# Kernel optimization log

Hardware: AMD Instinct MI355X
Metric: run time of the kernel (lower is better)

Reference implementation:

```python
import jax, jax.numpy as jnp
import numpy as np
import math

B, S, D, H = 4, 2048, 1024, 16
HD = D // H  # head_size = 64


def setup_inputs() -> dict:
    key = jax.random.key(0)
    ks = jax.random.split(key, 12)
    s = 1.0 / math.sqrt(D)
    inp = {
        "query_in": jax.random.normal(ks[0], (B, S, D), jnp.float32),
        "key_in": jax.random.normal(ks[1], (B, S, D), jnp.float32),
        "values_in": jax.random.normal(ks[2], (B, S, D), jnp.float32),
        # causal mask, broadcast over batch and heads
        "mask": jnp.tril(jnp.ones((S, S), jnp.int32))[None, None],
        "Wq": jax.random.normal(ks[3], (D, D), jnp.float32) * s,
        "bq": jnp.zeros((D,), jnp.float32),
        "Wk": jax.random.normal(ks[4], (D, D), jnp.float32) * s,
        "bk": jnp.zeros((D,), jnp.float32),
        "Wv": jax.random.normal(ks[5], (D, D), jnp.float32) * s,
        "bv": jnp.zeros((D,), jnp.float32),
        "Wo": jax.random.normal(ks[6], (D, D), jnp.float32) * s,
        "bo": jnp.zeros((D,), jnp.float32),
    }
    return inp


def _heads(x):
    # [B,S,D] -> [B,H,S,HD]
    return x.reshape(B, S, H, HD).transpose(0, 2, 1, 3)


def reference(query_in, key_in, values_in, mask, Wq, bq, Wk, bk, Wv, bv, Wo, bo):
    q = _heads(query_in @ Wq.T + bq)
    k = _heads(key_in @ Wk.T + bk)
    v = _heads(values_in @ Wv.T + bv)
    # scaled dot-product scores [B,H,Sq,Sk]
    att = jnp.einsum("bhqd,bhkd->bhqk", q, k) / math.sqrt(HD)
    att = jnp.where(mask == 0, jnp.float32(-1e9), att)
    # NOTE: original module applies dropout (identity at eval / p=0) directly
    # to scores with NO softmax -- faithfully reproduced here.
    out = jnp.einsum("bhqk,bhkd->bhqd", att, v)
    out = out.transpose(0, 2, 1, 3).reshape(B, S, D)
    return out @ Wo.T + bo
```

## Files before the change

kernel.cpp:

```cpp
#include <hip/hip_runtime.h>
#include <stdint.h>

typedef unsigned short ushort_t;
typedef __bf16 bf16x8 __attribute__((ext_vector_type(8)));
typedef float f32x4 __attribute__((ext_vector_type(4)));
typedef ushort_t us4 __attribute__((ext_vector_type(4)));

#define MFMA16(a, b, c) __builtin_amdgcn_mfma_f32_16x16x32_bf16((a), (b), (c), 0, 0, 0)

constexpr int Bn = 4, Sn = 2048, Dn = 1024, Hn = 16, HDn = 64;
constexpr float SCALE = 0.125f;
constexpr float NEG = -1e9f;

__device__ __forceinline__ float bf2f(ushort_t u) {
  unsigned x = ((unsigned)u) << 16;
  return __builtin_bit_cast(float, x);
}
__device__ __forceinline__ ushort_t f2bf(float f) {
  unsigned x = __builtin_bit_cast(unsigned, f);
  x = x + 0x7FFFu + ((x >> 16) & 1u);
  return (ushort_t)(x >> 16);
}
__device__ __forceinline__ uint4 ld8_f32_bf16(const float* __restrict__ p) {
  float4 a = *(const float4*)p;
  float4 b = *(const float4*)(p + 4);
  union { ushort_t u[8]; uint4 v; } r;
  r.u[0] = f2bf(a.x); r.u[1] = f2bf(a.y); r.u[2] = f2bf(a.z); r.u[3] = f2bf(a.w);
  r.u[4] = f2bf(b.x); r.u[5] = f2bf(b.y); r.u[6] = f2bf(b.z); r.u[7] = f2bf(b.w);
  return r.v;
}
__device__ __forceinline__ void gl2lds16(const void* g, void* l) {
  __builtin_amdgcn_global_load_lds(
      (__attribute__((address_space(1))) void*)g,
      (__attribute__((address_space(3))) void*)l, 16, 0, 0);
}

__global__ __launch_bounds__(256)
void cvt_all(const float* __restrict__ xq, const float* __restrict__ xk,
             const float* __restrict__ xv, const float* __restrict__ wq,
             const float* __restrict__ wk, const float* __restrict__ wv,
             const float* __restrict__ wo, ushort_t* __restrict__ Xd,
             ushort_t* __restrict__ Wd) {
  const int bid = blockIdx.x;
  if (bid < 12288) {
    const int which = bid >> 12;
    const float* s = which == 0 ? xq : which == 1 ? xk : xv;
    size_t i = ((size_t)(bid & 4095) * 256 + threadIdx.x) * 8;
    *(uint4*)(Xd + (size_t)which * 8388608 + i) = ld8_f32_bf16(s + i);
  } else {
    const int wb = bid - 12288, which = wb >> 9;
    const float* s = which == 0 ? wq : which == 1 ? wk : which == 2 ? wv : wo;
    size_t i = ((size_t)(wb & 511) * 256 + threadIdx.x) * 8;
    *(uint4*)(Wd + (size_t)which * 1048576 + i) = ld8_f32_bf16(s + i);
  }
}

__global__ __launch_bounds__(256, 4)
void gemm_qkv(const ushort_t* __restrict__ Xb, const ushort_t* __restrict__ Wb,
              const float* __restrict__ bq, const float* __restrict__ bk,
              const float* __restrict__ bv, ushort_t* __restrict__ Qd,
              ushort_t* __restrict__ Ktd, ushort_t* __restrict__ Vtd) {
  constexpr int K = 1024;
  __shared__ __align__(16) ushort_t As[128 * 64];
  __shared__ __align__(16) ushort_t Bs[128 * 64];

  const int z = blockIdx.z;
  const ushort_t* A  = Xb + (size_t)z * 8388608;
  const ushort_t* Wt = Wb + (size_t)z * 1048576;
  const float* bias = z == 0 ? bq : z == 1 ? bk : bv;
  ushort_t* Cp = z == 0 ? Qd : z == 1 ? Ktd : Vtd;

  const int tid = threadIdx.x;
  const int lane = tid & 63, w = tid >> 6;
  const int quad = lane >> 4, l16 = lane & 15;
  const int wm = w >> 1, wn = w & 1;
  const int row0 = blockIdx.x * 128;
  const int col0 = blockIdx.y * 128;

  const int sr = lane >> 3;
  const int sg = ((lane & 7) ^ (sr & 7)) * 8;
  const ushort_t* Ab = A  + (size_t)(row0 + w * 32 + sr) * K + sg;
  const ushort_t* Bb = Wt + (size_t)(col0 + w * 32 + sr) * K + sg;

  f32x4 acc[4][4] = {};

  for (int k0 = 0; k0 < K; k0 += 64) {
    __syncthreads();
#pragma unroll
    for (int i = 0; i < 4; ++i) {
      gl2lds16(Ab + (size_t)(i * 8) * K + k0, &As[(w * 32 + i * 8) * 64]);
      gl2lds16(Bb + (size_t)(i * 8) * K + k0, &Bs[(w * 32 + i * 8) * 64]);
    }
    __syncthreads();
#pragma unroll
    for (int ks = 0; ks < 2; ++ks) {
      const int kg = ((ks * 4 + quad) ^ (l16 & 7)) * 8;
      bf16x8 af[4], bfr[4];
#pragma unroll
      for (int mt = 0; mt < 4; ++mt)
        af[mt] = *(const bf16x8*)(&As[(wm * 64 + mt * 16 + l16) * 64 + kg]);
#pragma unroll
      for (int nt = 0; nt < 4; ++nt)
        bfr[nt] = *(const bf16x8*)(&Bs[(wn * 64 + nt * 16 + l16) * 64 + kg]);
#pragma unroll
      for (int mt = 0; mt < 4; ++mt)
#pragma unroll
        for (int nt = 0; nt < 4; ++nt)
          acc[mt][nt] = MFMA16(af[mt], bfr[nt], acc[mt][nt]);
    }
  }

#pragma unroll
  for (int mt = 0; mt < 4; ++mt) {
#pragma unroll
    for (int nt = 0; nt < 4; ++nt) {
      const int col = col0 + wn * 64 + nt * 16 + l16;
      const float bv4 = bias[col];
      const int rowb = row0 + wm * 64 + mt * 16 + quad * 4;
      if (z != 0) {
        const int b = rowb >> 11, s = rowb & (Sn - 1);
        const int h = col >> 6, hd = col & 63;
        us4 pk;
#pragma unroll
        for (int r = 0; r < 4; ++r) pk[r] = f2bf(acc[mt][nt][r] + bv4);
        *(us4*)(Cp + ((size_t)((b * Hn + h) * HDn + hd)) * Sn + s) = pk;
      } else {
#pragma unroll
        for (int r = 0; r < 4; ++r) {
          const int row = rowb + r;
          const int b = row >> 11, s = row & (Sn - 1);
          const int h = col >> 6, hd = col & 63;
          Cp[(((size_t)(b * Hn + h) * Sn + s) << 6) + hd] = f2bf(acc[mt][nt][r] + bv4);
        }
      }
    }
  }
}

__global__ __launch_bounds__(256, 4)
void gemm_out(const ushort_t* __restrict__ A, const ushort_t* __restrict__ Wt,
              const float* __restrict__ bias, float* __restrict__ Cp) {
  constexpr int K = 1024;
  __shared__ __align__(16) ushort_t As[128 * 64];
  __shared__ __align__(16) ushort_t Bs[128 * 64];

  const int tid = threadIdx.x;
  const int lane = tid & 63, w = tid >> 6;
  const int quad = lane >> 4, l16 = lane & 15;
  const int wm = w >> 1, wn = w & 1;
  const int row0 = blockIdx.x * 128;
  const int col0 = blockIdx.y * 128;

  const int sr = lane >> 3;
  const int sg = ((lane & 7) ^ (sr & 7)) * 8;
  const ushort_t* Ab = A  + (size_t)(row0 + w * 32 + sr) * K + sg;
  const ushort_t* Bb = Wt + (size_t)(col0 + w * 32 + sr) * K + sg;

  f32x4 acc[4][4] = {};

  for (int k0 = 0; k0 < K; k0 += 64) {
    __syncthreads();
#pragma unroll
    for (int i = 0; i < 4; ++i) {
      gl2lds16(Ab + (size_t)(i * 8) * K + k0, &As[(w * 32 + i * 8) * 64]);
      gl2lds16(Bb + (size_t)(i * 8) * K + k0, &Bs[(w * 32 + i * 8) * 64]);
    }
    __syncthreads();
#pragma unroll
    for (int ks = 0; ks < 2; ++ks) {
      const int kg = ((ks * 4 + quad) ^ (l16 & 7)) * 8;
      bf16x8 af[4], bfr[4];
#pragma unroll
      for (int mt = 0; mt < 4; ++mt)
        af[mt] = *(const bf16x8*)(&As[(wm * 64 + mt * 16 + l16) * 64 + kg]);
#pragma unroll
      for (int nt = 0; nt < 4; ++nt)
        bfr[nt] = *(const bf16x8*)(&Bs[(wn * 64 + nt * 16 + l16) * 64 + kg]);
#pragma unroll
      for (int mt = 0; mt < 4; ++mt)
#pragma unroll
        for (int nt = 0; nt < 4; ++nt)
          acc[mt][nt] = MFMA16(af[mt], bfr[nt], acc[mt][nt]);
    }
  }

#pragma unroll
  for (int mt = 0; mt < 4; ++mt)
#pragma unroll
    for (int nt = 0; nt < 4; ++nt) {
      const int col = col0 + wn * 64 + nt * 16 + l16;
      const float bv = bias[col];
      const int rowb = row0 + wm * 64 + mt * 16 + quad * 4;
#pragma unroll
      for (int r = 0; r < 4; ++r)
        Cp[(size_t)(rowb + r) * 1024 + col] = acc[mt][nt][r] + bv;
    }
}

__global__ __launch_bounds__(256)
void prefixz(const ushort_t* __restrict__ Kt, const ushort_t* __restrict__ Vt,
             ushort_t* __restrict__ Zp, float* __restrict__ suffV) {
  __shared__ __align__(16) ushort_t Kts[2][4096];
  __shared__ __align__(16) ushort_t Vts[2][4096];
  __shared__ float tsum[32 * 64];
  const int tid = threadIdx.x, lane = tid & 63, w = tid >> 6;
  const int quad = lane >> 4, l16 = lane & 15;
  const int bh = blockIdx.x;
  const ushort_t* Ktb = Kt + (size_t)bh * HDn * Sn;
  const ushort_t* Vtb = Vt + (size_t)bh * HDn * Sn;

  const int sr = lane >> 3;
  const int sg = ((lane & 7) ^ (sr & 7)) * 8;

  for (int i = tid; i < 2048; i += 256) tsum[i] = 0.f;

#pragma unroll
  for (int c = 0; c < 2; ++c) {
    const int row = w * 16 + c * 8;
    gl2lds16(Ktb + (size_t)(row + sr) * Sn + sg, &Kts[0][row * 64]);
    gl2lds16(Vtb + (size_t)(row + sr) * Sn + sg, &Vts[0][row * 64]);
  }

  f32x4 zacc[4] = {};

  for (int t = 0; t < 32; ++t) {
    const int cur = t & 1;
    __syncthreads();
    if (t < 31) {
#pragma unroll
      for (int c = 0; c < 2; ++c) {
        const int row = w * 16 + c * 8;
        gl2lds16(Ktb + (size_t)(row + sr) * Sn + (t + 1) * 64 + sg, &Kts[1 - cur][row * 64]);
        gl2lds16(Vtb + (size_t)(row + sr) * Sn + (t + 1) * 64 + sg, &Vts[1 - cur][row * 64]);
      }
    }
    ushort_t* zd = Zp + (size_t)(bh * 32 + t) * 4096;
#pragma unroll
    for (int nt = 0; nt < 4; ++nt) {
      us4 pk;
#pragma unroll
      for (int r = 0; r < 4; ++r) pk[r] = f2bf(SCALE * zacc[nt][r]);
      *(us4*)(zd + (nt * 16 + l16) * 64 + w * 16 + quad * 4) = pk;
    }
    if (t < 31) {
#pragma unroll
      for (int ks = 0; ks < 2; ++ks) {
        const int kg = ((ks * 4 + quad) ^ (l16 & 7)) * 8;
        bf16x8 ak = *(const bf16x8*)(&Kts[cur][(w * 16 + l16) * 64 + kg]);
#pragma unroll
        for (int nt = 0; nt < 4; ++nt) {
          bf16x8 bv8 = *(const bf16x8*)(&Vts[cur][(nt * 16 + l16) * 64 + kg]);
          zacc[nt] = MFMA16(ak, bv8, zacc[nt]);
        }
      }
    }
    {
      const int n = tid & 63, j = tid >> 6;
      float p = 0.f;
#pragma unroll
      for (int gg2 = 0; gg2 < 2; ++gg2) {
        const int g = 2 * j + gg2;
        union { uint4 v; ushort_t u[8]; } c;
        c.v = *(const uint4*)(&Vts[cur][n * 64 + ((g ^ (n & 7)) << 3)]);
#pragma unroll
        for (int e = 0; e < 8; ++e) p += bf2f(c.u[e]);
      }
      atomicAdd(&tsum[t * 64 + n], p);
    }
  }
  __syncthreads();
  if (tid < 64) {
    float acc = 0.f;
    for (int t = 31; t >= 0; --t) {
      suffV[(size_t)(bh * 32 + t) * 64 + tid] = acc;
      acc += tsum[t * 64 + tid];
    }
  }
}

__global__ __launch_bounds__(256)
void attn_kernel(const ushort_t* __restrict__ Q, const ushort_t* __restrict__ Kt,
                 const ushort_t* __restrict__ Vt, const ushort_t* __restrict__ Zp,
                 const float* __restrict__ suffV, ushort_t* __restrict__ O) {
  __shared__ __align__(16) ushort_t Qs[2][4096];
  __shared__ __align__(16) ushort_t Vts[2][4096];
  __shared__ __align__(16) ushort_t Zs[2][4096];
  __shared__ __align__(16) ushort_t Ks[2][4096];
  __shared__ __align__(16) ushort_t Ss[64][72];

  const int tid = threadIdx.x, lane = tid & 63, w = tid >> 6;
  const int quad = lane >> 4, l16 = lane & 15;
  const int bh = blockIdx.x;
  const int qtb = blockIdx.y * 4;
  const int b = bh >> 4, h = bh & 15;
  const ushort_t* Qb  = Q  + (size_t)bh * Sn * HDn;
  const ushort_t* Ktb = Kt + (size_t)bh * HDn * Sn;
  const ushort_t* Vtb = Vt + (size_t)bh * HDn * Sn;

  const int sr = lane >> 3;
  const int sg = ((lane & 7) ^ (sr & 7)) * 8;
  const int q8 = lane & 7, h8 = lane >> 3;

  uint4 kv[2];
  {
    const int q0 = qtb * 64;
    const ushort_t* Zb = Zp + (size_t)(bh * 32 + qtb) * 4096;
#pragma unroll
    for (int c = 0; c < 2; ++c) {
      const int row = w * 16 + c * 8;
      gl2lds16(Qb + (size_t)(q0 + row + sr) * HDn + sg, &Qs[0][row * 64]);
      gl2lds16(Vtb + (size_t)(row + sr) * Sn + q0 + sg, &Vts[0][row * 64]);
      gl2lds16(Zb + (size_t)(row + sr) * 64 + sg, &Zs[0][row * 64]);
      kv[c] = *(const uint4*)(Ktb + (size_t)(w * 16 + c * 8 + h8) * Sn + q0 + q8 * 8);
    }
  }

  for (int i = 0; i < 4; ++i) {
    const int cur = i & 1;
    const int qt = qtb + i, q0 = qt * 64;

#pragma unroll
    for (int c = 0; c < 2; ++c) {
      const int hd = w * 16 + c * 8 + h8;
      const int G = hd >> 3;
      const ushort_t* ku = (const ushort_t*)&kv[c];
#pragma unroll
      for (int j = 0; j < 8; ++j) {
        const int e = (j + q8) & 7;
        const int s = q8 * 8 + e;
        Ks[cur][s * 64 + ((G ^ e) << 3) + (hd & 7)] = ku[e];
      }
    }
    __syncthreads();

    if (i < 3) {
      const int q1 = (qt + 1) * 64;
      const ushort_t* Zb = Zp + (size_t)(bh * 32 + qt + 1) * 4096;
#pragma unroll
      for (int c = 0; c < 2; ++c) {
        const int row = w * 16 + c * 8;
        gl2lds16(Qb + (size_t)(q1 + row + sr) * HDn + sg, &Qs[1 - cur][row * 64]);
        gl2lds16(Vtb + (size_t)(row + sr) * Sn + q1 + sg, &Vts[1 - cur][row * 64]);
        gl2lds16(Zb + (size_t)(row + sr) * 64 + sg, &Zs[1 - cur][row * 64]);
        kv[c] = *(const uint4*)(Ktb + (size_t)(w * 16 + c * 8 + h8) * Sn + q1 + q8 * 8);
      }
    }

    bf16x8 bq[2];
#pragma unroll
    for (int ks = 0; ks < 2; ++ks)
      bq[ks] = *(const bf16x8*)(&Qs[cur][(w * 16 + l16) * 64 + (((ks * 4 + quad) ^ (l16 & 7)) << 3)]);

    f32x4 oacc[4] = {};
#pragma unroll
    for (int ks = 0; ks < 2; ++ks) {
      const int kg = ((ks * 4 + quad) ^ (l16 & 7)) * 8;
#pragma unroll
      for (int nt = 0; nt < 4; ++nt) {
        bf16x8 az = *(const bf16x8*)(&Zs[cur][(nt * 16 + l16) * 64 + kg]);
        oacc[nt] = MFMA16(az, bq[ks], oacc[nt]);
      }
    }
    f32x4 sacc[4] = {};
#pragma unroll
    for (int ks = 0; ks < 2; ++ks) {
      const int kg = ((ks * 4 + quad) ^ (l16 & 7)) * 8;
#pragma unroll
      for (int nt = 0; nt < 4; ++nt) {
        bf16x8 ak = *(const bf16x8*)(&Ks[cur][(nt * 16 + l16) * 64 + kg]);
        sacc[nt] = MFMA16(ak, bq[ks], sacc[nt]);
      }
    }
    const int qrel = w * 16 + l16;
#pragma unroll
    for (int nt = 0; nt < 4; ++nt) {
      const int kb = nt * 16 + quad * 4;
      us4 pk;
#pragma unroll
      for (int r = 0; r < 4; ++r) {
        float val = (kb + r > qrel) ? NEG : sacc[nt][r] * SCALE;
        pk[r] = f2bf(val);
      }
      *(us4*)(&Ss[qrel][kb]) = pk;
    }
#pragma unroll
    for (int ks = 0; ks < 2; ++ks) {
      bf16x8 bs = *(const bf16x8*)(&Ss[qrel][ks * 32 + quad * 8]);
#pragma unroll
      for (int nt = 0; nt < 4; ++nt) {
        bf16x8 av = *(const bf16x8*)(&Vts[cur][(nt * 16 + l16) * 64 + (((ks * 4 + quad) ^ (l16 & 7)) << 3)]);
        oacc[nt] = MFMA16(av, bs, oacc[nt]);
      }
    }

    const float* sv = suffV + (size_t)(bh * 32 + qt) * 64;
    const int s = q0 + w * 16 + l16;
#pragma unroll
    for (int nt = 0; nt < 4; ++nt) {
      const int nb = nt * 16 + quad * 4;
      float4 s4 = *(const float4*)(sv + nb);
      us4 pk;
      pk[0] = f2bf(oacc[nt][0] + NEG * s4.x);
      pk[1] = f2bf(oacc[nt][1] + NEG * s4.y);
      pk[2] = f2bf(oacc[nt][2] + NEG * s4.z);
      pk[3] = f2bf(oacc[nt][3] + NEG * s4.w);
      *(us4*)(&O[((size_t)(b * Sn + s)) * Dn + h * 64 + nb]) = pk;
    }
  }
}

extern "C" void kernel_launch(void* const* d_in, const int* in_sizes, int n_in,
                              void* d_out, int out_size, void* d_ws, size_t ws_size,
                              hipStream_t stream) {
  const float* Xq = (const float*)d_in[0];
  const float* Xk = (const float*)d_in[1];
  const float* Xv = (const float*)d_in[2];
  const float* Wq = (const float*)d_in[4];
  const float* bq = (const float*)d_in[5];
  const float* Wk = (const float*)d_in[6];
  const float* bk = (const float*)d_in[7];
  const float* Wv = (const float*)d_in[8];
  const float* bv = (const float*)d_in[9];
  const float* Wo = (const float*)d_in[10];
  const float* bo = (const float*)d_in[11];

  constexpr size_t MiB = 1024 * 1024;
  char* ws = (char*)d_ws;
  ushort_t* Xb  = (ushort_t*)(ws);
  ushort_t* Wb  = (ushort_t*)(ws + 48 * MiB);
  ushort_t* Qb  = (ushort_t*)(ws + 56 * MiB);
  ushort_t* Ktb = (ushort_t*)(ws + 72 * MiB);
  ushort_t* Vtb = (ushort_t*)(ws + 88 * MiB);
  ushort_t* Zp  = (ushort_t*)(ws + 104 * MiB);
  ushort_t* Ob  = (ushort_t*)(ws + 120 * MiB);
  float*    sV  = (float*)   (ws + 136 * MiB);

  cvt_all<<<14336, 256, 0, stream>>>(Xq, Xk, Xv, Wq, Wk, Wv, Wo, Xb, Wb);
  gemm_qkv<<<dim3(64, 8, 3), 256, 0, stream>>>(Xb, Wb, bq, bk, bv, Qb, Ktb, Vtb);
  prefixz<<<64, 256, 0, stream>>>(Ktb, Vtb, Zp, sV);
  attn_kernel<<<dim3(64, 8), 256, 0, stream>>>(Qb, Ktb, Vtb, Zp, sV, Ob);
  gemm_out<<<dim3(64, 8), 256, 0, stream>>>(Ob, Wb + (size_t)3 * 1048576, bo,
                                            (float*)d_out);
}
```

Before: 312.4 us.

## Split serial prefix kernel into parallel tile products plus scan, flatten attention grid

The single-block-per-head sequential prefix kernel, which looped over 32 key tiles on only 64 blocks, is replaced by a fully parallel per-tile K^T·V product kernel (2048 blocks) writing fp32 partials. A separate scan kernel then builds the exclusive prefix sums and the suffix V sums. The attention kernel now handles one query tile per block over a 64x32 grid instead of looping over four tiles with double buffering. This exposes far more parallelism in the serial stage, at the cost of an extra launch and an fp32 round trip through global memory for the partial products.

```diff
diff --git a/kernel.cpp b/kernel.cpp
--- a/kernel.cpp
+++ b/kernel.cpp
@@ -198,82 +198,96 @@
 }
 
 __global__ __launch_bounds__(256)
-void prefixz(const ushort_t* __restrict__ Kt, const ushort_t* __restrict__ Vt,
-             ushort_t* __restrict__ Zp, float* __restrict__ suffV) {
-  __shared__ __align__(16) ushort_t Kts[2][4096];
-  __shared__ __align__(16) ushort_t Vts[2][4096];
-  __shared__ float tsum[32 * 64];
+void gtile(const ushort_t* __restrict__ Kt, const ushort_t* __restrict__ Vt,
+           float* __restrict__ Gd, float* __restrict__ Rs) {
+  __shared__ __align__(16) ushort_t Kts[4096];
+  __shared__ __align__(16) ushort_t Vts[4096];
+  __shared__ float tsum[64];
   const int tid = threadIdx.x, lane = tid & 63, w = tid >> 6;
   const int quad = lane >> 4, l16 = lane & 15;
-  const int bh = blockIdx.x;
+  const int t = blockIdx.x, bh = blockIdx.y;
   const ushort_t* Ktb = Kt + (size_t)bh * HDn * Sn;
   const ushort_t* Vtb = Vt + (size_t)bh * HDn * Sn;
 
   const int sr = lane >> 3;
   const int sg = ((lane & 7) ^ (sr & 7)) * 8;
 
-  for (int i = tid; i < 2048; i += 256) tsum[i] = 0.f;
-
+  if (tid < 64) tsum[tid] = 0.f;
 #pragma unroll
   for (int c = 0; c < 2; ++c) {
     const int row = w * 16 + c * 8;
-    gl2lds16(Ktb + (size_t)(row + sr) * Sn + sg, &Kts[0][row * 64]);
-    gl2lds16(Vtb + (size_t)(row + sr) * Sn + sg, &Vts[0][row * 64]);
-  }
+    gl2lds16(Ktb + (size_t)(row + sr) * Sn + t * 64 + sg, &Kts[row * 64]);
+    gl2lds16(Vtb + (size_t)(row + sr) * Sn + t * 64 + sg, &Vts[row * 64]);
+  }
+  __syncthreads();
 
   f32x4 zacc[4] = {};
-
+#pragma unroll
+  for (int ks = 0; ks < 2; ++ks) {
+    const int kg = ((ks * 4 + quad) ^ (l16 & 7)) * 8;
+    bf16x8 ak = *(const bf16x8*)(&Kts[(w * 16 + l16) * 64 + kg]);
+#pragma unroll
+    for (int nt = 0; nt < 4; ++nt) {
+      bf16x8 bv8 = *(const bf16x8*)(&Vts[(nt * 16 + l16) * 64 + kg]);
+      zacc[nt] = MFMA16(ak, bv8, zacc[nt]);
+    }
+  }
+  float* gd = Gd + (size_t)(bh * 32 + t) * 4096;
+#pragma unroll
+  for (int nt = 0; nt < 4; ++nt)
+    *(f32x4*)(gd + (nt * 16 + l16) * 64 + w * 16 + quad * 4) = zacc[nt];
+
+  {
+    const int n = tid & 63, j = tid >> 6;
+    float p = 0.f;
+#pragma unroll
+    for (int gg2 = 0; gg2 < 2; ++gg2) {
+      const int g = 2 * j + gg2;
+      union { uint4 v; ushort_t u[8]; } c;
+      c.v = *(const uint4*)(&Vts[n * 64 + ((g ^ (n & 7)) << 3)]);
+#pragma unroll
+      for (int e = 0; e < 8; ++e) p += bf2f(c.u[e]);
+    }
+    atomicAdd(&tsum[n], p);
+  }
+  __syncthreads();
+  if (tid < 64) Rs[(size_t)(bh * 32 + t) * 64 + tid] = tsum[tid];
+}
+
+__global__ __launch_bounds__(256)
+void scanz(const float* __restrict__ Gd, const float* __restrict__ Rs,
+           ushort_t* __restrict__ Zp, float* __restrict__ suffV) {
+  const int tid = threadIdx.x;
+  const int nc = blockIdx.x, bh = blockIdx.y;
+  const int nl = tid >> 4;
+  const int n = nc * 16 + nl;
+  const int d0 = (tid & 15) * 4;
+  const float* gb = Gd + (size_t)bh * 32 * 4096 + n * 64 + d0;
+  ushort_t* zb = Zp + (size_t)bh * 32 * 4096 + n * 64 + d0;
+
+  f32x4 acc = {0.f, 0.f, 0.f, 0.f};
+  f32x4 g0 = *(const f32x4*)(gb);
+  f32x4 g1 = *(const f32x4*)(gb + 4096);
   for (int t = 0; t < 32; ++t) {
-    const int cur = t & 1;
-    __syncthreads();
-    if (t < 31) {
-#pragma unroll
-      for (int c = 0; c < 2; ++c) {
-        const int row = w * 16 + c * 8;
-        gl2lds16(Ktb + (size_t)(row + sr) * Sn + (t + 1) * 64 + sg, &Kts[1 - cur][row * 64]);
-        gl2lds16(Vtb + (size_t)(row + sr) * Sn + (t + 1) * 64 + sg, &Vts[1 - cur][row * 64]);
-      }
-    }
-    ushort_t* zd = Zp + (size_t)(bh * 32 + t) * 4096;
-#pragma unroll
-    for (int nt = 0; nt < 4; ++nt) {
-      us4 pk;
-#pragma unroll
-      for (int r = 0; r < 4; ++r) pk[r] = f2bf(SCALE * zacc[nt][r]);
-      *(us4*)(zd + (nt * 16 + l16) * 64 + w * 16 + quad * 4) = pk;
-    }
-    if (t < 31) {
-#pragma unroll
-      for (int ks = 0; ks < 2; ++ks) {
-        const int kg = ((ks * 4 + quad) ^ (l16 & 7)) * 8;
-        bf16x8 ak = *(const bf16x8*)(&Kts[cur][(w * 16 + l16) * 64 + kg]);
-#pragma unroll
-        for (int nt = 0; nt < 4; ++nt) {
-          bf16x8 bv8 = *(const bf16x8*)(&Vts[cur][(nt * 16 + l16) * 64 + kg]);
-          zacc[nt] = MFMA16(ak, bv8, zacc[nt]);
-        }
-      }
-    }
-    {
-      const int n = tid & 63, j = tid >> 6;
-      float p = 0.f;
-#pragma unroll
-      for (int gg2 = 0; gg2 < 2; ++gg2) {
-        const int g = 2 * j + gg2;
-        union { uint4 v; ushort_t u[8]; } c;
-        c.v = *(const uint4*)(&Vts[cur][n * 64 + ((g ^ (n & 7)) << 3)]);
-#pragma unroll
-        for (int e = 0; e < 8; ++e) p += bf2f(c.u[e]);
-      }
-      atomicAdd(&tsum[t * 64 + n], p);
-    }
-  }
+    us4 pk;
+#pragma unroll
+    for (int r = 0; r < 4; ++r) pk[r] = f2bf(SCALE * acc[r]);
+    *(us4*)(zb + (size_t)t * 4096) = pk;
+    const int tn = (t + 2 < 32) ? t + 2 : 31;
+    f32x4 gn = *(const f32x4*)(gb + (size_t)tn * 4096);
+    acc += g0;
+    g0 = g1; g1 = gn;
+  }
+
+  __shared__ float rs[32][16];
+  for (int i = tid; i < 512; i += 256)
+    rs[i >> 4][i & 15] = Rs[(size_t)(bh * 32 + (i >> 4)) * 64 + nc * 16 + (i & 15)];
   __syncthreads();
-  if (tid < 64) {
-    float acc = 0.f;
+  if (tid < 16) {
+    float a = 0.f;
     for (int t = 31; t >= 0; --t) {
-      suffV[(size_t)(bh * 32 + t) * 64 + tid] = acc;
-      acc += tsum[t * 64 + tid];
+      suffV[(size_t)(bh * 32 + t) * 64 + nc * 16 + tid] = a;
+      a += rs[t][tid];
     }
   }
 }
@@ -282,130 +296,110 @@
 void attn_kernel(const ushort_t* __restrict__ Q, const ushort_t* __restrict__ Kt,
                  const ushort_t* __restrict__ Vt, const ushort_t* __restrict__ Zp,
                  const float* __restrict__ suffV, ushort_t* __restrict__ O) {
-  __shared__ __align__(16) ushort_t Qs[2][4096];
-  __shared__ __align__(16) ushort_t Vts[2][4096];
-  __shared__ __align__(16) ushort_t Zs[2][4096];
-  __shared__ __align__(16) ushort_t Ks[2][4096];
+  __shared__ __align__(16) ushort_t Vts[4096];
+  __shared__ __align__(16) ushort_t Zs[4096];
+  __shared__ __align__(16) ushort_t Ks[4096];
   __shared__ __align__(16) ushort_t Ss[64][72];
 
   const int tid = threadIdx.x, lane = tid & 63, w = tid >> 6;
   const int quad = lane >> 4, l16 = lane & 15;
   const int bh = blockIdx.x;
-  const int qtb = blockIdx.y * 4;
+  const int qt = blockIdx.y, q0 = qt * 64;
   const int b = bh >> 4, h = bh & 15;
   const ushort_t* Qb  = Q  + (size_t)bh * Sn * HDn;
   const ushort_t* Ktb = Kt + (size_t)bh * HDn * Sn;
   const ushort_t* Vtb = Vt + (size_t)bh * HDn * Sn;
+  const ushort_t* Zb  = Zp + (size_t)(bh * 32 + qt) * 4096;
 
   const int sr = lane >> 3;
   const int sg = ((lane & 7) ^ (sr & 7)) * 8;
   const int q8 = lane & 7, h8 = lane >> 3;
 
   uint4 kv[2];
-  {
-    const int q0 = qtb * 64;
-    const ushort_t* Zb = Zp + (size_t)(bh * 32 + qtb) * 4096;
-#pragma unroll
-    for (int c = 0; c < 2; ++c) {
-      const int row = w * 16 + c * 8;
-      gl2lds16(Qb + (size_t)(q0 + row + sr) * HDn + sg, &Qs[0][row * 64]);
-      gl2lds16(Vtb + (size_t)(row + sr) * Sn + q0 + sg, &Vts[0][row * 64]);
-      gl2lds16(Zb + (size_t)(row + sr) * 64 + sg, &Zs[0][row * 64]);
-      kv[c] = *(const uint4*)(Ktb + (size_t)(w * 16 + c * 8 + h8) * Sn + q0 + q8 * 8);
-    }
-  }
-
-  for (int i = 0; i < 4; ++i) {
-    const int cur = i & 1;
-    const int qt = qtb + i, q0 = qt * 64;
-
-#pragma unroll
-    for (int c = 0; c < 2; ++c) {
-      const int hd = w * 16 + c * 8 + h8;
-      const int G = hd >> 3;
-      const ushort_t* ku = (const ushort_t*)&kv[c];
-#pragma unroll
-      for (int j = 0; j < 8; ++j) {
-        const int e = (j + q8) & 7;
-        const int s = q8 * 8 + e;
-        Ks[cur][s * 64 + ((G ^ e) << 3) + (hd & 7)] = ku[e];
-      }
-    }
-    __syncthreads();
-
-    if (i < 3) {
-      const int q1 = (qt + 1) * 64;
-      const ushort_t* Zb = Zp + (size_t)(bh * 32 + qt + 1) * 4096;
-#pragma unroll
-      for (int c = 0; c < 2; ++c) {
-        const int row = w * 16 + c * 8;
-        gl2lds16(Qb + (size_t)(q1 + row + sr) * HDn + sg, &Qs[1 - cur][row * 64]);
-        gl2lds16(Vtb + (size_t)(row + sr) * Sn + q1 + sg, &Vts[1 - cur][row * 64]);
-        gl2lds16(Zb + (size_t)(row + sr) * 64 + sg, &Zs[1 - cur][row * 64]);
-        kv[c] = *(const uint4*)(Ktb + (size_t)(w * 16 + c * 8 + h8) * Sn + q1 + q8 * 8);
-      }
-    }
-
-    bf16x8 bq[2];
-#pragma unroll
-    for (int ks = 0; ks < 2; ++ks)
-      bq[ks] = *(const bf16x8*)(&Qs[cur][(w * 16 + l16) * 64 + (((ks * 4 + quad) ^ (l16 & 7)) << 3)]);
-
-    f32x4 oacc[4] = {};
-#pragma unroll
-    for (int ks = 0; ks < 2; ++ks) {
-      const int kg = ((ks * 4 + quad) ^ (l16 & 7)) * 8;
-#pragma unroll
-      for (int nt = 0; nt < 4; ++nt) {
-        bf16x8 az = *(const bf16x8*)(&Zs[cur][(nt * 16 + l16) * 64 + kg]);
-        oacc[nt] = MFMA16(az, bq[ks], oacc[nt]);
-      }
-    }
-    f32x4 sacc[4] = {};
-#pragma unroll
-    for (int ks = 0; ks < 2; ++ks) {
-      const int kg = ((ks * 4 + quad) ^ (l16 & 7)) * 8;
-#pragma unroll
-      for (int nt = 0; nt < 4; ++nt) {
-        bf16x8 ak = *(const bf16x8*)(&Ks[cur][(nt * 16 + l16) * 64 + kg]);
-        sacc[nt] = MFMA16(ak, bq[ks], sacc[nt]);
-      }
-    }
-    const int qrel = w * 16 + l16;
-#pragma unroll
-    for (int nt = 0; nt < 4; ++nt) {
-      const int kb = nt * 16 + quad * 4;
-      us4 pk;
-#pragma unroll
-      for (int r = 0; r < 4; ++r) {
-        float val = (kb + r > qrel) ? NEG : sacc[nt][r] * SCALE;
-        pk[r] = f2bf(val);
-      }
-      *(us4*)(&Ss[qrel][kb]) = pk;
-    }
-#pragma unroll
-    for (int ks = 0; ks < 2; ++ks) {
-      bf16x8 bs = *(const bf16x8*)(&Ss[qrel][ks * 32 + quad * 8]);
-#pragma unroll
-      for (int nt = 0; nt < 4; ++nt) {
-        bf16x8 av = *(const bf16x8*)(&Vts[cur][(nt * 16 + l16) * 64 + (((ks * 4 + quad) ^ (l16 & 7)) << 3)]);
-        oacc[nt] = MFMA16(av, bs, oacc[nt]);
-      }
-    }
-
-    const float* sv = suffV + (size_t)(bh * 32 + qt) * 64;
-    const int s = q0 + w * 16 + l16;
-#pragma unroll
-    for (int nt = 0; nt < 4; ++nt) {
-      const int nb = nt * 16 + quad * 4;
-      float4 s4 = *(const float4*)(sv + nb);
-      us4 pk;
-      pk[0] = f2bf(oacc[nt][0] + NEG * s4.x);
-      pk[1] = f2bf(oacc[nt][1] + NEG * s4.y);
-      pk[2] = f2bf(oacc[nt][2] + NEG * s4.z);
-      pk[3] = f2bf(oacc[nt][3] + NEG * s4.w);
-      *(us4*)(&O[((size_t)(b * Sn + s)) * Dn + h * 64 + nb]) = pk;
-    }
+#pragma unroll
+  for (int c = 0; c < 2; ++c)
+    kv[c] = *(const uint4*)(Ktb + (size_t)(w * 16 + c * 8 + h8) * Sn + q0 + q8 * 8);
+
+#pragma unroll
+  for (int c = 0; c < 2; ++c) {
+    const int row = w * 16 + c * 8;
+    gl2lds16(Vtb + (size_t)(row + sr) * Sn + q0 + sg, &Vts[row * 64]);
+    gl2lds16(Zb + (size_t)(row + sr) * 64 + sg, &Zs[row * 64]);
+  }
+
+  bf16x8 bq[2];
+#pragma unroll
+  for (int ks = 0; ks < 2; ++ks)
+    bq[ks] = *(const bf16x8*)(Qb + (size_t)(q0 + w * 16 + l16) * HDn + (ks * 4 + quad) * 8);
+
+#pragma unroll
+  for (int c = 0; c < 2; ++c) {
+    const int hd = w * 16 + c * 8 + h8;
+    const int G = hd >> 3;
+    const ushort_t* ku = (const ushort_t*)&kv[c];
+#pragma unroll
+    for (int j = 0; j < 8; ++j) {
+      const int e = (j + q8) & 7;
+      const int s = q8 * 8 + e;
+      Ks[s * 64 + ((G ^ e) << 3) + (hd & 7)] = ku[e];
+    }
+  }
+  __syncthreads();
+
+  f32x4 oacc[4] = {};
+#pragma unroll
+  for (int ks = 0; ks < 2; ++ks) {
+    const int kg = ((ks * 4 + quad) ^ (l16 & 7)) * 8;
+#pragma unroll
+    for (int nt = 0; nt < 4; ++nt) {
+      bf16x8 az = *(const bf16x8*)(&Zs[(nt * 16 + l16) * 64 + kg]);
+      oacc[nt] = MFMA16(az, bq[ks], oacc[nt]);
+    }
+  }
+  f32x4 sacc[4] = {};
+#pragma unroll
+  for (int ks = 0; ks < 2; ++ks) {
+    const int kg = ((ks * 4 + quad) ^ (l16 & 7)) * 8;
+#pragma unroll
+    for (int nt = 0; nt < 4; ++nt) {
+      bf16x8 ak = *(const bf16x8*)(&Ks[(nt * 16 + l16) * 64 + kg]);
+      sacc[nt] = MFMA16(ak, bq[ks], sacc[nt]);
+    }
+  }
+  const int qrel = w * 16 + l16;
+#pragma unroll
+  for (int nt = 0; nt < 4; ++nt) {
+    const int kb = nt * 16 + quad * 4;
+    us4 pk;
+#pragma unroll
+    for (int r = 0; r < 4; ++r) {
+      float val = (kb + r > qrel) ? NEG : sacc[nt][r] * SCALE;
+      pk[r] = f2bf(val);
+    }
+    *(us4*)(&Ss[qrel][kb]) = pk;
+  }
+#pragma unroll
+  for (int ks = 0; ks < 2; ++ks) {
+    bf16x8 bs = *(const bf16x8*)(&Ss[qrel][ks * 32 + quad * 8]);
+#pragma unroll
+    for (int nt = 0; nt < 4; ++nt) {
+      bf16x8 av = *(const bf16x8*)(&Vts[(nt * 16 + l16) * 64 + (((ks * 4 + quad) ^ (l16 & 7)) << 3)]);
+      oacc[nt] = MFMA16(av, bs, oacc[nt]);
+    }
+  }
+
+  const float* sv = suffV + (size_t)(bh * 32 + qt) * 64;
+  const int s = q0 + w * 16 + l16;
+#pragma unroll
+  for (int nt = 0; nt < 4; ++nt) {
+    const int nb = nt * 16 + quad * 4;
+    float4 s4 = *(const float4*)(sv + nb);
+    us4 pk;
+    pk[0] = f2bf(oacc[nt][0] + NEG * s4.x);
+    pk[1] = f2bf(oacc[nt][1] + NEG * s4.y);
+    pk[2] = f2bf(oacc[nt][2] + NEG * s4.z);
+    pk[3] = f2bf(oacc[nt][3] + NEG * s4.w);
+    *(us4*)(&O[((size_t)(b * Sn + s)) * Dn + h * 64 + nb]) = pk;
   }
 }
 
@@ -434,11 +428,14 @@
   ushort_t* Zp  = (ushort_t*)(ws + 104 * MiB);
   ushort_t* Ob  = (ushort_t*)(ws + 120 * MiB);
   float*    sV  = (float*)   (ws + 136 * MiB);
+  float*    Gd  = (float*)   (ws + 144 * MiB);
+  float*    Rsum= (float*)   (ws + 176 * MiB);
 
   cvt_all<<<14336, 256, 0, stream>>>(Xq, Xk, Xv, Wq, Wk, Wv, Wo, Xb, Wb);
   gemm_qkv<<<dim3(64, 8, 3), 256, 0, stream>>>(Xb, Wb, bq, bk, bv, Qb, Ktb, Vtb);
-  prefixz<<<64, 256, 0, stream>>>(Ktb, Vtb, Zp, sV);
-  attn_kernel<<<dim3(64, 8), 256, 0, stream>>>(Qb, Ktb, Vtb, Zp, sV, Ob);
+  gtile<<<dim3(32, 64), 256, 0, stream>>>(Ktb, Vtb, Gd, Rsum);
+  scanz<<<dim3(4, 64), 256, 0, stream>>>(Gd, Rsum, Zp, sV);
+  attn_kernel<<<dim3(64, 32), 256, 0, stream>>>(Qb, Ktb, Vtb, Zp, sV, Ob);
   gemm_out<<<dim3(64, 8), 256, 0, stream>>>(Ob, Wb + (size_t)3 * 1048576, bo,
                                             (float*)d_out);
 }
```

Result: faster. 298.1 us (-4.6%).
